# Performance work log

Measured on AMD Instinct MI355X. Metric: run time of the kernel, lower is better.

Reference implementation:

```python
import jax, jax.numpy as jnp
import numpy as np

N, B, C, H, E = 1024, 4, 256, 4, 32768
D = C // H  # head_dim = 64


def setup_inputs() -> dict:
    key = jax.random.key(0)
    ks = jax.random.split(key, 16)
    p = lambda k, shape: (jax.random.normal(k, shape) * 0.05).astype(jnp.float32)
    return {
        "x": jax.random.normal(ks[0], (N, B, C), jnp.float32),
        "edge_features": jax.random.normal(ks[1], (N, N, C), jnp.float32),
        "src_idx": jax.random.randint(ks[2], (E,), 0, N, jnp.int32),
        "trg_idx": jax.random.randint(ks[3], (E,), 0, N, jnp.int32),
        "Wn1": p(ks[4], (C, C)), "We1": p(ks[5], (C, C)),
        "a_src1": p(ks[6], (H, D)), "a_tgt1": p(ks[7], (H, D)),
        "a_edge1": jnp.ones((H,), jnp.float32),
        "Wn2": p(ks[8], (C, C)), "We2": p(ks[9], (C, C)),
        "a_src2": p(ks[10], (H, D)), "a_tgt2": p(ks[11], (H, D)),
        "a_edge2": jnp.ones((H,), jnp.float32),
    }


def _gat_layer(x, e_feats, src, trg, Wn, We, a_s, a_t, a_e):
    # x: [N,B,C], e_feats: [E,C] (gathered edge features)
    n, b, _ = x.shape
    h = (x @ Wn.T).reshape(n, b, H, D)          # node projection, all batches at once
    h_src = h[src]                              # [E,B,H,D]
    h_tgt = h[trg]                              # [E,B,H,D]
    s = (jnp.einsum('ebhd,hd->ebh', h_src, a_s)
         + jnp.einsum('ebhd,hd->ebh', h_tgt, a_t))          # [E,B,H]
    pe = ((e_feats @ We.T).reshape(-1, H, D).sum(-1) * a_e)  # [E,H], batch-independent
    scores = jax.nn.leaky_relu(s + pe[:, None, :], negative_slope=0.2)
    exp_s = jnp.exp(scores)                                  # faithful to exp/scatter softmax
    denom = jax.ops.segment_sum(exp_s, trg, num_segments=n)  # [N,B,H]
    attn = exp_s / (denom[trg] + 1e-16)                      # [E,B,H]
    out = jax.ops.segment_sum(h_src * attn[..., None], trg, num_segments=n)  # [N,B,H,D]
    return out.reshape(n, b, H * D)


def reference(x, edge_features, src_idx, trg_idx,
              Wn1, We1, a_src1, a_tgt1, a_edge1,
              Wn2, We2, a_src2, a_tgt2, a_edge2):
    e_feats = edge_features[src_idx, trg_idx]  # [E,C], same raw edge feats feed both layers
    x1 = _gat_layer(x, e_feats, src_idx, trg_idx, Wn1, We1, a_src1, a_tgt1, a_edge1)
    x2 = _gat_layer(x1, e_feats, src_idx, trg_idx, Wn2, We2, a_src2, a_tgt2, a_edge2)
    return x2
```

## Files before the change

kernel.cpp:

```cpp
#include <hip/hip_runtime.h>
#include <cstdint>
#include <cstddef>

#define NN 1024
#define BB 4
#define CC 256
#define HH 4
#define DD 64
#define EE 32768
#define ROWS 8
#define CAP 128
#define NTHR 256

struct Params {
    const float *x, *ef;
    const int *src, *trg;
    const float *Wn1, *We1, *as1, *at1, *ae1;
    const float *Wn2, *We2, *as2, *at2, *ae2;
    float *out;
    float *WnT1, *WnT2, *wsum, *pe, *hbuf, *alphas, *alphat;
    float *hbuf2, *alphas2, *alphat2;
    int *cnt, *bucket;
};

__device__ __forceinline__ void proj_body(const float* __restrict__ x,
                                          const float* __restrict__ WT,
                                          const float* __restrict__ a_s,
                                          const float* __restrict__ a_t,
                                          float* __restrict__ hout,
                                          float* __restrict__ alpha_s,
                                          float* __restrict__ alpha_t,
                                          int bid, int t) {
    int r0 = bid * ROWS;
    const float* xr = x + (size_t)r0 * CC;
    float acc[ROWS];
#pragma unroll
    for (int j = 0; j < ROWS; ++j) acc[j] = 0.f;
#pragma unroll 4
    for (int c = 0; c < CC; ++c) {
        float w = WT[c * CC + t];
#pragma unroll
        for (int j = 0; j < ROWS; ++j) acc[j] += w * xr[(size_t)j * CC + c];
    }
    int h = t >> 6, d = t & 63;
    float as = a_s[h * DD + d], at = a_t[h * DD + d];
#pragma unroll
    for (int j = 0; j < ROWS; ++j) {
        hout[(size_t)(r0 + j) * CC + t] = acc[j];
        float vs = acc[j] * as, vt = acc[j] * at;
#pragma unroll
        for (int off = 32; off; off >>= 1) {
            vs += __shfl_down(vs, off, 64);
            vt += __shfl_down(vt, off, 64);
        }
        if (d == 0) {
            alpha_s[(size_t)(r0 + j) * HH + h] = vs;
            alpha_t[(size_t)(r0 + j) * HH + h] = vt;
        }
    }
}

__device__ __forceinline__ void sort_bucket(const Params& p, int n, int deg, int lane,
                                            int* sed) {
    if (deg <= 64) {
        int v = (lane < deg) ? p.bucket[n * CAP + lane] : 0x7fffffff;
        int rank = 0;
#pragma unroll
        for (int j = 0; j < 64; ++j) {
            int vj = __shfl(v, j, 64);
            rank += (vj < v) ? 1 : 0;
        }
        if (lane < deg) sed[rank] = v;
    } else if (lane == 0) {
        for (int i = 0; i < deg; ++i) sed[i] = p.bucket[n * CAP + i];
        for (int i = 1; i < deg; ++i) {
            int v = sed[i], j = i - 1;
            while (j >= 0 && sed[j] > v) { sed[j + 1] = sed[j]; --j; }
            sed[j + 1] = v;
        }
    }
}

__device__ __forceinline__ void stage_edges(const Params& p, const float* __restrict__ pe_l,
                                            const float* __restrict__ als, int t, int deg,
                                            const int* sed, int* ssrc,
                                            float (*spe)[HH], float (*sals)[16]) {
    if (t < deg) {
        int e = sed[t];
        int s = p.src[e];
        ssrc[t] = s;
        *(float4*)spe[t] = *(const float4*)(pe_l + (size_t)e * HH);
        const float4* ap = (const float4*)(als + (size_t)s * 16);
        float4* dp = (float4*)sals[t];
        dp[0] = ap[0]; dp[1] = ap[1]; dp[2] = ap[2]; dp[3] = ap[3];
    }
}

__global__ __launch_bounds__(NTHR) void k_prep(Params p) {
    __shared__ float tile[64][65];
    int bid = blockIdx.x, t = threadIdx.x;
    if (bid < 32) {
        int m = bid >> 4, tl = bid & 15, ti = tl >> 2, tj = tl & 3;
        const float* W = m ? p.Wn2 : p.Wn1;
        float* WT = m ? p.WnT2 : p.WnT1;
#pragma unroll
        for (int k = 0; k < 16; ++k) {
            int idx = k * 256 + t, r = idx >> 6, c = idx & 63;
            tile[r][c] = W[(ti * 64 + r) * CC + tj * 64 + c];
        }
        __syncthreads();
#pragma unroll
        for (int k = 0; k < 16; ++k) {
            int idx = k * 256 + t, r = idx >> 6, c = idx & 63;
            WT[(tj * 64 + r) * CC + ti * 64 + c] = tile[c][r];
        }
    } else if (bid < 40) {
        int idx = (bid - 32) * 256 + t;
        int l = idx >> 10, h = (idx >> 8) & 3, c = idx & 255;
        const float* We = l ? p.We2 : p.We1;
        const float* ae = l ? p.ae2 : p.ae1;
        float s = 0.f;
        for (int d = 0; d < DD; ++d) s += We[(h * DD + d) * CC + c];
        p.wsum[(l * HH + h) * CC + c] = s * ae[h];
    } else {
        p.cnt[(bid - 40) * 256 + t] = 0;
    }
}

__global__ __launch_bounds__(NTHR) void k_main1(Params p) {
    int bid = blockIdx.x, t = threadIdx.x;
    if (bid < 128) {
        int e = bid * NTHR + t;
        int n = p.trg[e];
        int pos = atomicAdd(&p.cnt[n], 1);
        if (pos < CAP) p.bucket[n * CAP + pos] = e;
    } else if (bid < 640) {
        proj_body(p.x, p.WnT1, p.as1, p.at1, p.hbuf, p.alphas, p.alphat, bid - 128, t);
    } else {
        int pb = bid - 640, wid = t >> 6, lane = t & 63;
        float4 wv[8];
#pragma unroll
        for (int i = 0; i < 8; ++i)
            wv[i] = *(const float4*)(p.wsum + i * CC + lane * 4);
        int e0 = pb * 16 + wid * 4;
        int4 s4 = *(const int4*)(p.src + e0);
        int4 g4 = *(const int4*)(p.trg + e0);
        int se[4] = {s4.x, s4.y, s4.z, s4.w};
        int ge[4] = {g4.x, g4.y, g4.z, g4.w};
        float4 v[4];
#pragma unroll
        for (int k = 0; k < 4; ++k)
            v[k] = *(const float4*)(p.ef + ((long)se[k] * NN + ge[k]) * CC + lane * 4);
#pragma unroll
        for (int k = 0; k < 4; ++k) {
            float acc[8];
#pragma unroll
            for (int i = 0; i < 8; ++i)
                acc[i] = v[k].x * wv[i].x + v[k].y * wv[i].y + v[k].z * wv[i].z
                       + v[k].w * wv[i].w;
#pragma unroll
            for (int off = 32; off; off >>= 1)
#pragma unroll
                for (int i = 0; i < 8; ++i) acc[i] += __shfl_down(acc[i], off, 64);
            if (lane == 0) {
                int e = e0 + k;
                *(float4*)(p.pe + (size_t)e * HH) =
                    make_float4(acc[0], acc[1], acc[2], acc[3]);
                *(float4*)(p.pe + (size_t)EE * HH + (size_t)e * HH) =
                    make_float4(acc[4], acc[5], acc[6], acc[7]);
            }
        }
    }
}

__global__ __launch_bounds__(NTHR) void k_fuse1(Params p) {
    __shared__ int sedge[CAP];
    __shared__ int ssrc[CAP];
    __shared__ float spe[CAP][HH];
    __shared__ float sals[CAP][16];
    __shared__ float x1s[4][CC];
    __shared__ int sdeg;
    int n = blockIdx.x, t = threadIdx.x, b = t >> 6, lane = t & 63;
    int deg = p.cnt[n];
    if (deg > CAP) deg = CAP;
    if (b == 0) {
        if (lane == 0) sdeg = deg;
        sort_bucket(p, n, deg, lane, sedge);
    }
    __syncthreads();
    stage_edges(p, p.pe, p.alphas, t, deg, sedge, ssrc, spe, sals);
    __syncthreads();

    int h = lane >> 4;
    float at_n = p.alphat[(size_t)n * 16 + b * 4 + h];
    float ax = 0.f, ay = 0.f, az = 0.f, aw = 0.f, den = 0.f;
#pragma unroll 4
    for (int i = 0; i < deg; ++i) {
        int s = ssrc[i];
        float sc = sals[i][b * 4 + h] + at_n + spe[i][h];
        sc = sc > 0.f ? sc : 0.2f * sc;
        float ex = __expf(sc);
        float4 v = *(const float4*)(p.hbuf + ((size_t)s * BB + b) * CC + lane * 4);
        ax += ex * v.x; ay += ex * v.y; az += ex * v.z; aw += ex * v.w;
        den += ex;
    }
    float inv = 1.f / (den + 1e-16f);
    *(float4*)&x1s[b][lane * 4] = make_float4(ax * inv, ay * inv, az * inv, aw * inv);
    __syncthreads();

    float acc[4];
#pragma unroll
    for (int r = 0; r < 4; ++r) acc[r] = 0.f;
#pragma unroll 4
    for (int c = 0; c < CC; ++c) {
        float w = p.WnT2[c * CC + t];
#pragma unroll
        for (int r = 0; r < 4; ++r) acc[r] += w * x1s[r][c];
    }
    int hh = t >> 6, d = t & 63;
    float as = p.as2[hh * DD + d], at = p.at2[hh * DD + d];
#pragma unroll
    for (int r = 0; r < 4; ++r) {
        p.hbuf2[((size_t)n * BB + r) * CC + t] = acc[r];
        float vs = acc[r] * as, vt = acc[r] * at;
#pragma unroll
        for (int off = 32; off; off >>= 1) {
            vs += __shfl_down(vs, off, 64);
            vt += __shfl_down(vt, off, 64);
        }
        if (d == 0) {
            p.alphas2[(size_t)n * 16 + r * 4 + hh] = vs;
            p.alphat2[(size_t)n * 16 + r * 4 + hh] = vt;
        }
    }
}

__global__ __launch_bounds__(NTHR) void k_agg2(Params p) {
    __shared__ int sedge[CAP];
    __shared__ int ssrc[CAP];
    __shared__ float spe[CAP][HH];
    __shared__ float sals[CAP][16];
    __shared__ int sdeg;
    int n = blockIdx.x, t = threadIdx.x, b = t >> 6, lane = t & 63;
    int deg = p.cnt[n];
    if (deg > CAP) deg = CAP;
    if (b == 0) {
        if (lane == 0) sdeg = deg;
        sort_bucket(p, n, deg, lane, sedge);
    }
    __syncthreads();
    stage_edges(p, p.pe + (size_t)EE * HH, p.alphas2, t, deg, sedge, ssrc, spe, sals);
    __syncthreads();

    int h = lane >> 4;
    float at_n = p.alphat2[(size_t)n * 16 + b * 4 + h];
    float ax = 0.f, ay = 0.f, az = 0.f, aw = 0.f, den = 0.f;
#pragma unroll 4
    for (int i = 0; i < deg; ++i) {
        int s = ssrc[i];
        float sc = sals[i][b * 4 + h] + at_n + spe[i][h];
        sc = sc > 0.f ? sc : 0.2f * sc;
        float ex = __expf(sc);
        float4 v = *(const float4*)(p.hbuf2 + ((size_t)s * BB + b) * CC + lane * 4);
        ax += ex * v.x; ay += ex * v.y; az += ex * v.z; aw += ex * v.w;
        den += ex;
    }
    float inv = 1.f / (den + 1e-16f);
    *(float4*)(p.out + ((size_t)n * BB + b) * CC + lane * 4) =
        make_float4(ax * inv, ay * inv, az * inv, aw * inv);
}

extern "C" void kernel_launch(void* const* d_in, const int* in_sizes, int n_in,
                              void* d_out, int out_size, void* d_ws, size_t ws_size,
                              hipStream_t stream) {
    float* wsf = (float*)d_ws;
    Params p;
    p.x   = (const float*)d_in[0];
    p.ef  = (const float*)d_in[1];
    p.src = (const int*)d_in[2];
    p.trg = (const int*)d_in[3];
    p.Wn1 = (const float*)d_in[4];
    p.We1 = (const float*)d_in[5];
    p.as1 = (const float*)d_in[6];
    p.at1 = (const float*)d_in[7];
    p.ae1 = (const float*)d_in[8];
    p.Wn2 = (const float*)d_in[9];
    p.We2 = (const float*)d_in[10];
    p.as2 = (const float*)d_in[11];
    p.at2 = (const float*)d_in[12];
    p.ae2 = (const float*)d_in[13];
    p.out = (float*)d_out;
    p.WnT1    = wsf;
    p.WnT2    = wsf + 65536;
    p.wsum    = wsf + 131072;
    p.pe      = wsf + 133120;
    p.hbuf    = wsf + 395264;
    p.alphas  = wsf + 1443840;
    p.alphat  = wsf + 1460224;
    p.hbuf2   = wsf + 1476608;
    p.alphas2 = wsf + 2525184;
    p.alphat2 = wsf + 2541568;
    p.cnt     = (int*)(wsf + 2557952);
    p.bucket  = (int*)(wsf + 2557952 + 1024);

    k_prep<<<44, NTHR, 0, stream>>>(p);
    k_main1<<<2688, NTHR, 0, stream>>>(p);
    k_fuse1<<<NN, NTHR, 0, stream>>>(p);
    k_agg2<<<NN, NTHR, 0, stream>>>(p);
}
```

Measured before the change: 108.5 us.

## Precompute edge softmax exponents once per edge and reuse sorted edge lists

Both aggregation kernels now compute each edge's leaky-relu score and exponential once per (edge, batch, head) in a parallel pre-pass into shared memory. Previously these were computed redundantly by every one of the 16 lanes sharing a head inside the serial aggregation loop. The layer-1 kernel also writes its sorted edge and source lists to workspace, so the layer-2 kernel reads them instead of re-sorting the bucket. This adds a workspace write/read, an extra barrier, and more shared memory. The aggregation loop unroll is also raised from 4 to 8.

```diff
diff --git a/kernel.cpp b/kernel.cpp
--- a/kernel.cpp
+++ b/kernel.cpp
@@ -20,7 +20,7 @@
     float *out;
     float *WnT1, *WnT2, *wsum, *pe, *hbuf, *alphas, *alphat;
     float *hbuf2, *alphas2, *alphat2;
-    int *cnt, *bucket;
+    int *cnt, *bucket, *sedge_g, *ssrc_g;
 };
 
 __device__ __forceinline__ void proj_body(const float* __restrict__ x,
@@ -81,18 +81,20 @@
     }
 }
 
-__device__ __forceinline__ void stage_edges(const Params& p, const float* __restrict__ pe_l,
-                                            const float* __restrict__ als, int t, int deg,
-                                            const int* sed, int* ssrc,
-                                            float (*spe)[HH], float (*sals)[16]) {
-    if (t < deg) {
-        int e = sed[t];
-        int s = p.src[e];
-        ssrc[t] = s;
-        *(float4*)spe[t] = *(const float4*)(pe_l + (size_t)e * HH);
-        const float4* ap = (const float4*)(als + (size_t)s * 16);
-        float4* dp = (float4*)sals[t];
-        dp[0] = ap[0]; dp[1] = ap[1]; dp[2] = ap[2]; dp[3] = ap[3];
+__device__ __forceinline__ void score_exp(const float* __restrict__ als,
+                                          const float* salt, int t, int deg,
+                                          const int* ssrc, const float (*spe)[HH],
+                                          float (*sex)[16]) {
+#pragma unroll
+    for (int k = 0; k < 8; ++k) {
+        int idx = k * NTHR + t;
+        if (idx < deg * 16) {
+            int i = idx >> 4, bh = idx & 15;
+            int s = ssrc[i];
+            float sc = als[(size_t)s * 16 + bh] + salt[bh] + spe[i][bh & 3];
+            sc = sc > 0.f ? sc : 0.2f * sc;
+            sex[i][bh] = __expf(sc);
+        }
     }
 }
 
@@ -177,7 +179,8 @@
     __shared__ int sedge[CAP];
     __shared__ int ssrc[CAP];
     __shared__ float spe[CAP][HH];
-    __shared__ float sals[CAP][16];
+    __shared__ float sex[CAP][16];
+    __shared__ float salt[16];
     __shared__ float x1s[4][CC];
     __shared__ int sdeg;
     int n = blockIdx.x, t = threadIdx.x, b = t >> 6, lane = t & 63;
@@ -187,20 +190,26 @@
         if (lane == 0) sdeg = deg;
         sort_bucket(p, n, deg, lane, sedge);
     }
-    __syncthreads();
-    stage_edges(p, p.pe, p.alphas, t, deg, sedge, ssrc, spe, sals);
-    __syncthreads();
-
-    int h = lane >> 4;
-    float at_n = p.alphat[(size_t)n * 16 + b * 4 + h];
+    if (t < 16) salt[t] = p.alphat[(size_t)n * 16 + t];
+    __syncthreads();
+    if (t < deg) {
+        int e = sedge[t];
+        int s = p.src[e];
+        ssrc[t] = s;
+        *(float4*)spe[t] = *(const float4*)(p.pe + (size_t)e * HH);
+        p.sedge_g[n * CAP + t] = e;
+        p.ssrc_g[n * CAP + t] = s;
+    }
+    __syncthreads();
+    score_exp(p.alphas, salt, t, deg, ssrc, spe, sex);
+    __syncthreads();
+
+    int h = lane >> 4, bh = b * 4 + h;
     float ax = 0.f, ay = 0.f, az = 0.f, aw = 0.f, den = 0.f;
-#pragma unroll 4
+#pragma unroll 8
     for (int i = 0; i < deg; ++i) {
-        int s = ssrc[i];
-        float sc = sals[i][b * 4 + h] + at_n + spe[i][h];
-        sc = sc > 0.f ? sc : 0.2f * sc;
-        float ex = __expf(sc);
-        float4 v = *(const float4*)(p.hbuf + ((size_t)s * BB + b) * CC + lane * 4);
+        float ex = sex[i][bh];
+        float4 v = *(const float4*)(p.hbuf + ((size_t)ssrc[i] * BB + b) * CC + lane * 4);
         ax += ex * v.x; ay += ex * v.y; az += ex * v.z; aw += ex * v.w;
         den += ex;
     }
@@ -236,32 +245,29 @@
 }
 
 __global__ __launch_bounds__(NTHR) void k_agg2(Params p) {
-    __shared__ int sedge[CAP];
     __shared__ int ssrc[CAP];
     __shared__ float spe[CAP][HH];
-    __shared__ float sals[CAP][16];
-    __shared__ int sdeg;
+    __shared__ float sex[CAP][16];
+    __shared__ float salt[16];
     int n = blockIdx.x, t = threadIdx.x, b = t >> 6, lane = t & 63;
     int deg = p.cnt[n];
     if (deg > CAP) deg = CAP;
-    if (b == 0) {
-        if (lane == 0) sdeg = deg;
-        sort_bucket(p, n, deg, lane, sedge);
-    }
-    __syncthreads();
-    stage_edges(p, p.pe + (size_t)EE * HH, p.alphas2, t, deg, sedge, ssrc, spe, sals);
-    __syncthreads();
-
-    int h = lane >> 4;
-    float at_n = p.alphat2[(size_t)n * 16 + b * 4 + h];
+    if (t < 16) salt[t] = p.alphat2[(size_t)n * 16 + t];
+    if (t < deg) {
+        int e = p.sedge_g[n * CAP + t];
+        ssrc[t] = p.ssrc_g[n * CAP + t];
+        *(float4*)spe[t] = *(const float4*)(p.pe + (size_t)EE * HH + (size_t)e * HH);
+    }
+    __syncthreads();
+    score_exp(p.alphas2, salt, t, deg, ssrc, spe, sex);
+    __syncthreads();
+
+    int h = lane >> 4, bh = b * 4 + h;
     float ax = 0.f, ay = 0.f, az = 0.f, aw = 0.f, den = 0.f;
-#pragma unroll 4
+#pragma unroll 8
     for (int i = 0; i < deg; ++i) {
-        int s = ssrc[i];
-        float sc = sals[i][b * 4 + h] + at_n + spe[i][h];
-        sc = sc > 0.f ? sc : 0.2f * sc;
-        float ex = __expf(sc);
-        float4 v = *(const float4*)(p.hbuf2 + ((size_t)s * BB + b) * CC + lane * 4);
+        float ex = sex[i][bh];
+        float4 v = *(const float4*)(p.hbuf2 + ((size_t)ssrc[i] * BB + b) * CC + lane * 4);
         ax += ex * v.x; ay += ex * v.y; az += ex * v.z; aw += ex * v.w;
         den += ex;
     }
@@ -302,6 +308,8 @@
     p.alphat2 = wsf + 2541568;
     p.cnt     = (int*)(wsf + 2557952);
     p.bucket  = (int*)(wsf + 2557952 + 1024);
+    p.sedge_g = (int*)(wsf + 2557952 + 1024 + NN * CAP);
+    p.ssrc_g  = (int*)(wsf + 2557952 + 1024 + 2 * NN * CAP);
 
     k_prep<<<44, NTHR, 0, stream>>>(p);
     k_main1<<<2688, NTHR, 0, stream>>>(p);
```

Measured after the change: 109.4 us. About the same (+0.8%).
